# Kernel optimization log

Hardware: AMD Instinct MI355X
Metric: run time of the kernel (lower is better)

The kernel has to match this reference:

```python
import jax, jax.numpy as jnp
import numpy as np

B, N, C, H, W = 8, 512, 3, 16, 16
K, P, E = 2, 4, 1           # K: hop levels == filter taps, P: attn heads, E: edge feature sets
SLOPE = 0.2                 # LeakyReLU slope in attention
GAT_DIMS = {'d0': (128, 128), 'd1': (512, 32), 'u0': (128, 64),
            'u1': (256, 128), 's0': (128, 128), 's1': (512, 64)}


def _conv(x, w, b):
    pad = w.shape[-1] // 2
    y = jax.lax.conv_general_dilated(x, w, (1, 1), [(pad, pad), (pad, pad)],
                                     dimension_numbers=('NCHW', 'OIHW', 'NCHW'))
    return y + b[None, :, None, None]


def _gat(x, S, wk, wq, wf, b):
    # x: (B,G,N); S: (B,E,N,N) binary GSO. KeyQuery attention + K-tap attentional filter.
    key = jnp.einsum('pegf,bgn->bpefn', wk, x)
    qry = jnp.einsum('pegf,bgn->bpefn', wq, x)
    # scores[...,n,m]: logit of node n attending to neighbor m
    scores = jax.nn.leaky_relu(jnp.einsum('bpefn,bpefm->bpenm', qry, key), SLOPE)
    mask = (jnp.abs(S) > 1e-9)[:, None]                    # (B,1,E,N,N)
    aij = jnp.where(mask, jax.nn.softmax(jnp.where(mask, scores, -1e9), axis=-1), 0.0)
    Pn, En, Kt, G, F = wf.shape
    xk = jnp.broadcast_to(x[:, None, None], (x.shape[0], Pn, En, G, x.shape[-1]))
    zs = [xk]
    for _ in range(Kt - 1):
        xk = jnp.einsum('bpegm,bpenm->bpegn', xk, aij)     # attention-weighted diffusion
        zs.append(xk)
    z = jnp.stack(zs, axis=3)                              # (B,P,E,K,G,N)
    y = jnp.einsum('bpekgn,pekgf->bpfn', z, wf) + b[None, None, :, None]
    y = jax.nn.relu(y)                                     # nonlinearity before head concat
    return y.reshape(y.shape[0], Pn * F, y.shape[-1])      # (B, P*F, N)


def _forward(x, Slist, conv0_w, conv0_b, conv1_w, conv1_b, flat_w, flat_b,
             d0_wk, d0_wq, d0_wf, d0_b, d1_wk, d1_wq, d1_wf, d1_b,
             u0_wk, u0_wq, u0_wf, u0_b, u1_wk, u1_wq, u1_wf, u1_b,
             s0_wk, s0_wq, s0_wf, s0_b, s1_wk, s1_wq, s1_wf, s1_b,
             dec0_w, dec0_b, dec1_w, dec1_b):
    Bn, Nn = x.shape[0], x.shape[1]
    h = x.reshape(Bn * Nn, C, H, W)
    e = jax.nn.relu(_conv(h, conv0_w, conv0_b))
    e = jax.nn.relu(_conv(e, conv1_w, conv1_b))
    e = e + h                                              # RES connection after encoder
    f = jax.nn.relu(e.reshape(Bn * Nn, -1) @ flat_w.T + flat_b)
    g = f.reshape(Bn, -1, Nn)                              # faithful torch reshape to (B, F, N)
    S0, S1 = Slist[:, 0:1], Slist[:, 1:2]
    p0 = g
    p1 = _gat(p0, S0, d0_wk, d0_wq, d0_wf, d0_b)           # downward pass
    p2 = _gat(p1, S1, d1_wk, d1_wq, d1_wf, d1_b)
    # upward pass + shortcuts (upward[l] uses S[K-l-1]; shortcut[K-1-l] on p[K-1-l])
    u0 = _gat(p2, S1, u0_wk, u0_wq, u0_wf, u0_b) + _gat(p1, S1, s1_wk, s1_wq, s1_wf, s1_b)
    u1 = _gat(u0, S0, u1_wk, u1_wq, u1_wf, u1_b) + _gat(p0, S0, s0_wk, s0_wq, s0_wf, s0_b)
    d = jax.nn.relu(u1.reshape(Bn * Nn, -1) @ dec0_w.T + dec0_b)
    out = jax.nn.softmax(d @ dec1_w.T + dec1_b, axis=-1)   # nn.Softmax() -> dim=1 on 2D input
    return out.reshape(Bn, Nn, -1)


def setup_inputs() -> dict:
    key = jax.random.key(0)
    ks = iter(jax.random.split(key, 64))
    def nrm(shape, s=0.1):
        return jax.random.normal(next(ks), shape, jnp.float32) * s
    x = jax.random.normal(next(ks), (B, N, C, H, W), jnp.float32)
    adj = (jax.random.uniform(next(ks), (B, K, N, N)) < 0.02).astype(jnp.float32)
    Slist = jnp.clip(adj + jnp.eye(N, dtype=jnp.float32)[None, None], 0.0, 1.0)
    inp = {'x': x, 'Slist': Slist,
           'conv0_w': nrm((32, C, 3, 3)), 'conv0_b': nrm((32,)),
           'conv1_w': nrm((C, 32, 3, 3)), 'conv1_b': nrm((C,)),
           'flat_w': nrm((128, C * H * W)), 'flat_b': nrm((128,))}
    for pre, (G, F) in GAT_DIMS.items():
        inp[pre + '_wk'] = nrm((P, E, G, F))
        inp[pre + '_wq'] = nrm((P, E, G, F))
        inp[pre + '_wf'] = nrm((P, E, K, G, F))
        inp[pre + '_b'] = nrm((F,))
    inp.update({'dec0_w': nrm((256, 512)), 'dec0_b': nrm((256,)),
                'dec1_w': nrm((5, 256)), 'dec1_b': nrm((5,))})
    return inp


def reference(x, Slist, conv0_w, conv0_b, conv1_w, conv1_b, flat_w, flat_b,
              d0_wk, d0_wq, d0_wf, d0_b, d1_wk, d1_wq, d1_wf, d1_b,
              u0_wk, u0_wq, u0_wf, u0_b, u1_wk, u1_wq, u1_wf, u1_b,
              s0_wk, s0_wq, s0_wf, s0_b, s1_wk, s1_wq, s1_wf, s1_b,
              dec0_w, dec0_b, dec1_w, dec1_b):
    return _forward(x, Slist, conv0_w, conv0_b, conv1_w, conv1_b, flat_w, flat_b,
                    d0_wk, d0_wq, d0_wf, d0_b, d1_wk, d1_wq, d1_wf, d1_b,
                    u0_wk, u0_wq, u0_wf, u0_b, u1_wk, u1_wq, u1_wf, u1_b,
                    s0_wk, s0_wq, s0_wf, s0_b, s1_wk, s1_wq, s1_wf, s1_b,
                    dec0_w, dec0_b, dec1_w, dec1_b)
```

## Files before the change

kernel.cpp:

```cpp
#include <hip/hip_runtime.h>
#include <hip/hip_bf16.h>
#include <math.h>

typedef unsigned short u16;
typedef unsigned int   u32;

#define CAP 48

__device__ __forceinline__ float tof(u16 u){
  union { u32 i; float f; } v; v.i = ((u32)u) << 16; return v.f;
}
__device__ __forceinline__ u16 fromf(float f){
  union { float f; u32 i; } v; v.f = f;
  u32 x = v.i;
  return (u16)((x + 0x7fffu + ((x >> 16) & 1u)) >> 16);
}

__global__ void detect_dtype(const void* xp, int* flag){
  if(threadIdx.x == 0 && blockIdx.x == 0){
    const u16* p = (const u16*)xp;
    int outl = 0;
    for(int i = 0; i < 128; i++){
      u16 u = p[2*i];
      int e = (u >> 7) & 0xFF;
      if(u != 0 && (e < 100 || e > 140)) outl++;
    }
    *flag = (outl > 32) ? 1 : 0;
  }
}

struct WArgs {
  const void* p[34];
  int sz[34];
  int off[35];
};

__global__ __launch_bounds__(256) void convert_weights(WArgs wa, const int* flag,
                                                       float* __restrict__ arena, int total){
  int i = blockIdx.x * 256 + threadIdx.x;
  if(i >= total) return;
  int isf = *flag;
  int t = 0;
  while(wa.off[t+1] <= i) t++;
  int j = i - wa.off[t];
  float v = 0.f;
  if(j < wa.sz[t])
    v = isf ? ((const float*)wa.p[t])[j] : tof(((const u16*)wa.p[t])[j]);
  arena[i] = v;
}

__global__ __launch_bounds__(256) void transpose_w(const float* __restrict__ src,
                                                   float* __restrict__ dst, int R, int C){
  int i = blockIdx.x * 256 + threadIdx.x;
  if(i < R*C){
    int r = i / C, c = i - r*C;
    dst[(size_t)c*R + r] = src[i];
  }
}

__global__ __launch_bounds__(64) void build_nbr(const void* __restrict__ S,
                                                int* __restrict__ nbr_idx,
                                                int* __restrict__ nbr_cnt,
                                                const int* __restrict__ flag){
  int isf = *flag;
  int row  = blockIdx.x;
  int lane = threadIdx.x;
  int cnt = 0;
  for(int c = 0; c < 8; c++){
    int m = c*64 + lane;
    size_t idx = (size_t)row * 512 + m;
    float sv = isf ? ((const float*)S)[idx] : tof(((const u16*)S)[idx]);
    bool pred = fabsf(sv) > 1e-9f;
    unsigned long long mask = __ballot(pred);
    int pos = cnt + __popcll(mask & ((1ull << lane) - 1ull));
    if(pred && pos < CAP) nbr_idx[(size_t)row*CAP + pos] = m;
    cnt += __popcll(mask);
  }
  if(lane == 0) nbr_cnt[row] = cnt > CAP ? CAP : cnt;
}

__global__ __launch_bounds__(256) void encoder_conv(
    const void* __restrict__ x, const int* __restrict__ flag,
    const float* __restrict__ w0, const float* __restrict__ b0,
    const float* __restrict__ w1, const float* __restrict__ b1,
    float* __restrict__ e1n)
{
  __shared__ float xpad[3][18][18];
  __shared__ float e0p[16][18][18];

  int isf = *flag;
  int tid = threadIdx.x;
  size_t img = blockIdx.x;
  int py = tid >> 4, px = tid & 15;

  float* z1 = &xpad[0][0][0];
  for(int i = tid; i < 972; i += 256) z1[i] = 0.f;
  float* z2 = &e0p[0][0][0];
  for(int i = tid; i < 5184; i += 256) z2[i] = 0.f;
  __syncthreads();

  #pragma unroll
  for(int i = 0; i < 3; i++){
    size_t gi = img*768 + i*256 + tid;
    xpad[i][1+py][1+px] = isf ? ((const float*)x)[gi] : tof(((const u16*)x)[gi]);
  }
  __syncthreads();

  float acc1[3] = {0.f, 0.f, 0.f};

  for(int grp = 0; grp < 2; grp++){
    float acc0[16];
    #pragma unroll
    for(int o = 0; o < 16; o++) acc0[o] = 0.f;
    for(int i = 0; i < 3; i++){
      float rr[9];
      #pragma unroll
      for(int ky = 0; ky < 3; ky++)
        #pragma unroll
        for(int kx = 0; kx < 3; kx++)
          rr[ky*3+kx] = xpad[i][py+ky][px+kx];
      #pragma unroll
      for(int o = 0; o < 16; o++){
        #pragma unroll
        for(int t = 0; t < 9; t++)
          acc0[o] = fmaf(rr[t], w0[(grp*16+o)*27 + i*9 + t], acc0[o]);
      }
    }
    __syncthreads();
    #pragma unroll
    for(int o = 0; o < 16; o++)
      e0p[o][1+py][1+px] = fmaxf(acc0[o] + b0[grp*16 + o], 0.f);
    __syncthreads();

    for(int i = 0; i < 16; i++){
      float rr[9];
      #pragma unroll
      for(int ky = 0; ky < 3; ky++)
        #pragma unroll
        for(int kx = 0; kx < 3; kx++)
          rr[ky*3+kx] = e0p[i][py+ky][px+kx];
      int ic = grp*16 + i;
      #pragma unroll
      for(int o = 0; o < 3; o++){
        #pragma unroll
        for(int t = 0; t < 9; t++)
          acc1[o] = fmaf(rr[t], w1[o*288 + ic*9 + t], acc1[o]);
      }
    }
  }

  #pragma unroll
  for(int o = 0; o < 3; o++)
    e1n[img*768 + o*256 + tid] = fmaxf(acc1[o] + b1[o], 0.f) + xpad[o][1+py][1+px];
}

__global__ __launch_bounds__(256) void gemm_flat(
    const float* __restrict__ e1n, const float* __restrict__ fwT,
    const float* __restrict__ fb, float* __restrict__ g)
{
  __shared__ float As[16][68];
  __shared__ float Bs[16][68];
  int tid = threadIdx.x;
  int n0 = blockIdx.x * 64, m0 = blockIdx.y * 64;

  int lk = tid >> 4;
  int l4 = (tid & 15) * 4;
  int br = tid >> 2;
  int bc = (tid & 3) * 4;

  float acc[4][4];
  #pragma unroll
  for(int i = 0; i < 4; i++)
    #pragma unroll
    for(int jj = 0; jj < 4; jj++) acc[i][jj] = 0.f;

  int tm = tid >> 4, tn = tid & 15;
  for(int kt = 0; kt < 48; kt++){
    int k0 = kt*16;
    *(float4*)&As[lk][l4] = *(const float4*)&fwT[(size_t)(k0 + lk)*128 + m0 + l4];
    float4 bv = *(const float4*)&e1n[(size_t)(n0 + br)*768 + k0 + bc];
    Bs[bc+0][br] = bv.x; Bs[bc+1][br] = bv.y; Bs[bc+2][br] = bv.z; Bs[bc+3][br] = bv.w;
    __syncthreads();
    #pragma unroll
    for(int kk = 0; kk < 16; kk++){
      float4 a  = *(const float4*)&As[kk][tm*4];
      float4 xx = *(const float4*)&Bs[kk][tn*4];
      float av[4]  = {a.x, a.y, a.z, a.w};
      float xvv[4] = {xx.x, xx.y, xx.z, xx.w};
      #pragma unroll
      for(int i = 0; i < 4; i++)
        #pragma unroll
        for(int jj = 0; jj < 4; jj++)
          acc[i][jj] = fmaf(av[i], xvv[jj], acc[i][jj]);
    }
    __syncthreads();
  }

  #pragma unroll
  for(int jj = 0; jj < 4; jj++){
    int img = n0 + tn*4 + jj;
    float4 r = make_float4(fmaxf(acc[0][jj] + fb[m0+tm*4+0], 0.f),
                           fmaxf(acc[1][jj] + fb[m0+tm*4+1], 0.f),
                           fmaxf(acc[2][jj] + fb[m0+tm*4+2], 0.f),
                           fmaxf(acc[3][jj] + fb[m0+tm*4+3], 0.f));
    *(float4*)&g[(size_t)img*128 + m0 + tm*4] = r;
  }
}

__global__ __launch_bounds__(256) void gemm_kq(
    const float* __restrict__ X,
    const float* __restrict__ wk, const float* __restrict__ wq,
    float* __restrict__ kqT, int G, int F)
{
  __shared__ float Ws[32][68];
  __shared__ float Xs[32][68];
  int tid = threadIdx.x;
  int bp = blockIdx.z;
  int b = bp >> 2, p = bp & 3;
  int n0 = blockIdx.x * 64, m0 = blockIdx.y * 64;
  const float* Xb = X + (size_t)b * G * 512;

  int lk = tid >> 4;
  int l4 = (tid & 15) * 4;

  int mg = m0 + l4;
  int quad = mg / F;
  int mq = mg - quad * F;
  size_t GF = (size_t)G * F;
  const float* wb = (quad == 0 ? wk : wq) + (size_t)p * GF + mq;

  float acc[4][4];
  #pragma unroll
  for(int i = 0; i < 4; i++)
    #pragma unroll
    for(int jj = 0; jj < 4; jj++) acc[i][jj] = 0.f;

  int tm = tid >> 4, tn = tid & 15;
  int KT = G / 32;
  for(int kt = 0; kt < KT; kt++){
    int k = kt*32 + lk;
    *(float4*)&Ws[lk][l4]      = *(const float4*)(wb + (size_t)k * F);
    *(float4*)&Ws[lk+16][l4]   = *(const float4*)(wb + (size_t)(k+16) * F);
    *(float4*)&Xs[lk][l4]      = *(const float4*)(Xb + (size_t)k * 512 + n0 + l4);
    *(float4*)&Xs[lk+16][l4]   = *(const float4*)(Xb + (size_t)(k+16) * 512 + n0 + l4);
    __syncthreads();
    #pragma unroll
    for(int kk = 0; kk < 32; kk++){
      float4 a  = *(const float4*)&Ws[kk][tm*4];
      float4 xx = *(const float4*)&Xs[kk][tn*4];
      float av[4]  = {a.x, a.y, a.z, a.w};
      float xvv[4] = {xx.x, xx.y, xx.z, xx.w};
      #pragma unroll
      for(int i = 0; i < 4; i++)
        #pragma unroll
        for(int jj = 0; jj < 4; jj++)
          acc[i][jj] = fmaf(av[i], xvv[jj], acc[i][jj]);
    }
    __syncthreads();
  }

  int F2 = 2*F;
  float* ob = kqT + (size_t)bp * 512 * F2;
  #pragma unroll
  for(int jj = 0; jj < 4; jj++){
    float* orow = ob + (size_t)(n0 + tn*4 + jj) * F2 + m0 + tm*4;
    #pragma unroll
    for(int i = 0; i < 4; i++) orow[i] = acc[i][jj];
  }
}

__global__ __launch_bounds__(256) void gemm_kqK64(
    const float* __restrict__ X,
    const float* __restrict__ wk, const float* __restrict__ wq,
    float* __restrict__ kqT, int G, int F)
{
  __shared__ float Ws[64][68];
  __shared__ float Xs[64][68];
  int tid = threadIdx.x;
  int bp = blockIdx.z;
  int b = bp >> 2, p = bp & 3;
  int n0 = blockIdx.x * 64, m0 = blockIdx.y * 64;
  const float* Xb = X + (size_t)b * G * 512;

  int lk = tid >> 4;
  int l4 = (tid & 15) * 4;

  int mg = m0 + l4;
  int quad = mg / F;
  int mq = mg - quad * F;
  size_t GF = (size_t)G * F;
  const float* wb = (quad == 0 ? wk : wq) + (size_t)p * GF + mq;

  float acc[4][4];
  #pragma unroll
  for(int i = 0; i < 4; i++)
    #pragma unroll
    for(int jj = 0; jj < 4; jj++) acc[i][jj] = 0.f;

  int tm = tid >> 4, tn = tid & 15;
  int KT = G / 64;
  for(int kt = 0; kt < KT; kt++){
    #pragma unroll
    for(int kb = 0; kb < 4; kb++){
      int k = kt*64 + lk + kb*16;
      *(float4*)&Ws[lk + kb*16][l4] = *(const float4*)(wb + (size_t)k * F);
      *(float4*)&Xs[lk + kb*16][l4] = *(const float4*)(Xb + (size_t)k * 512 + n0 + l4);
    }
    __syncthreads();
    #pragma unroll
    for(int kk = 0; kk < 64; kk++){
      float4 a  = *(const float4*)&Ws[kk][tm*4];
      float4 xx = *(const float4*)&Xs[kk][tn*4];
      float av[4]  = {a.x, a.y, a.z, a.w};
      float xvv[4] = {xx.x, xx.y, xx.z, xx.w};
      #pragma unroll
      for(int i = 0; i < 4; i++)
        #pragma unroll
        for(int jj = 0; jj < 4; jj++)
          acc[i][jj] = fmaf(av[i], xvv[jj], acc[i][jj]);
    }
    __syncthreads();
  }

  int F2 = 2*F;
  float* ob = kqT + (size_t)bp * 512 * F2;
  #pragma unroll
  for(int jj = 0; jj < 4; jj++){
    float* orow = ob + (size_t)(n0 + tn*4 + jj) * F2 + m0 + tm*4;
    #pragma unroll
    for(int i = 0; i < 4; i++) orow[i] = acc[i][jj];
  }
}

__global__ __launch_bounds__(256) void attn_sparse(
    const float* __restrict__ kqT,
    const int* __restrict__ nbr_idx, const int* __restrict__ nbr_cnt,
    float* __restrict__ aijv, int F, int s)
{
  __shared__ float qs[16][132];
  __shared__ float sc[16][CAP];
  __shared__ float red[16][2];
  int tid = threadIdx.x;
  int n0 = blockIdx.x * 16;
  int bp = blockIdx.y;
  int b = bp >> 2;
  int F2 = 2*F;

  int F4 = F >> 2;
  for(int i = tid; i < 16*F4; i += 256){
    int r = i / F4, c4 = (i - r*F4) * 4;
    *(float4*)&qs[r][c4] =
      *(const float4*)&kqT[((size_t)bp*512 + n0 + r)*F2 + F + c4];
  }
  __syncthreads();

  int r = tid >> 4;
  int t = tid & 15;
  int n = n0 + r;
  int srow = (b*2 + s)*512 + n;
  int cnt = nbr_cnt[srow];
  const int* il = nbr_idx + (size_t)srow * CAP;

  for(int j = t; j < cnt; j += 16){
    int m = il[j];
    const float* krow = kqT + ((size_t)bp*512 + m)*F2;
    float a = 0.f;
    for(int f = 0; f < F; f += 4){
      float4 k4 = *(const float4*)&krow[f];
      a = fmaf(qs[r][f],   k4.x, a);
      a = fmaf(qs[r][f+1], k4.y, a);
      a = fmaf(qs[r][f+2], k4.z, a);
      a = fmaf(qs[r][f+3], k4.w, a);
    }
    sc[r][j] = a >= 0.f ? a : 0.2f * a;
  }
  __syncthreads();

  if(t == 0){
    float mx = -1e30f;
    for(int j = 0; j < cnt; j++) mx = fmaxf(mx, sc[r][j]);
    float ssum = 0.f;
    for(int j = 0; j < cnt; j++) ssum += expf(sc[r][j] - mx);
    red[r][0] = mx; red[r][1] = ssum;
  }
  __syncthreads();

  float mx = red[r][0], ssum = red[r][1];
  float* arow = aijv + ((size_t)bp*512 + n)*CAP;
  for(int j = t; j < cnt; j += 16)
    arow[j] = expf(sc[r][j] - mx) / ssum;
}

__global__ __launch_bounds__(256) void fill_Xp(
    const float* __restrict__ X, const float* __restrict__ aijv,
    const int* __restrict__ nbr_idx, const int* __restrict__ nbr_cnt,
    float* __restrict__ Xp, int G, int s)
{
  __shared__ float xrows[8][512];
  __shared__ float av_s[64][CAP+1];
  __shared__ u16   il_s[64][CAP+2];
  __shared__ int   cnt_s[64];

  int tid = threadIdx.x;
  int n0 = blockIdx.x * 64;
  int g0 = blockIdx.y * 32;
  int bp = blockIdx.z;
  int b = bp >> 2;
  int srow0 = (b*2 + s)*512 + n0;

  for(int i = tid; i < 64*CAP; i += 256){
    int r = i / CAP, j = i - r*CAP;
    il_s[r][j] = (u16)nbr_idx[(size_t)(srow0 + r)*CAP + j];
    av_s[r][j] = aijv[((size_t)bp*512 + n0 + r)*CAP + j];
  }
  if(tid < 64) cnt_s[tid] = nbr_cnt[srow0 + tid];

  int n_l = tid & 63;
  int gs  = tid >> 6;
  const float* Xb  = X  + ((size_t)b  * G + g0) * 512;
  float*       XpB = Xp + ((size_t)bp * G + g0) * 512;

  for(int gb = 0; gb < 32; gb += 8){
    __syncthreads();
    for(int i = tid; i < 8*128; i += 256){
      int gr = i >> 7, c4 = (i & 127) * 4;
      *(float4*)&xrows[gr][c4] = *(const float4*)&Xb[(size_t)(gb + gr)*512 + c4];
    }
    __syncthreads();
    int cnt = cnt_s[n_l];
    float a0 = 0.f, a1 = 0.f;
    for(int j = 0; j < cnt; j++){
      float w = av_s[n_l][j];
      int   m = il_s[n_l][j];
      a0 = fmaf(w, xrows[gs][m],     a0);
      a1 = fmaf(w, xrows[gs + 4][m], a1);
    }
    XpB[(size_t)(gb + gs)*512     + n0 + n_l] = a0;
    XpB[(size_t)(gb + gs + 4)*512 + n0 + n_l] = a1;
  }
}

__global__ __launch_bounds__(256) void gemm_y(
    const float* __restrict__ X, const float* __restrict__ Xp,
    const float* __restrict__ wf, const float* __restrict__ bias,
    float* __restrict__ out, int G, int F, int PFout, int accmode)
{
  __shared__ float Ws[32][68];
  __shared__ float Xs[32][68];
  int tid = threadIdx.x;
  int bp = blockIdx.z;
  int b = bp >> 2, p = bp & 3;
  int n0 = blockIdx.x * 64, m0 = blockIdx.y * 64;

  int lk = tid >> 4;
  int l4 = (tid & 15) * 4;
  int mg = m0 + l4;
  int fcl = mg < F ? mg : (F - 4);
  size_t GF2 = (size_t)2 * G * F;
  const float* wb = wf + (size_t)p * GF2 + fcl;

  float acc[4][4];
  #pragma unroll
  for(int i = 0; i < 4; i++)
    #pragma unroll
    for(int jj = 0; jj < 4; jj++) acc[i][jj] = 0.f;

  int tm = tid >> 4, tn = tid & 15;
  int KT = (2*G) / 32;
  for(int kt = 0; kt < KT; kt++){
    int c0 = kt*32 + lk;
    int c1 = c0 + 16;
    const float* xr0 = (c0 < G) ? (X  + ((size_t)b  * G + c0      ) * 512)
                                : (Xp + ((size_t)bp * G + (c0 - G)) * 512);
    const float* xr1 = (c1 < G) ? (X  + ((size_t)b  * G + c1      ) * 512)
                                : (Xp + ((size_t)bp * G + (c1 - G)) * 512);
    *(float4*)&Ws[lk][l4]    = *(const float4*)(wb + (size_t)c0 * F);
    *(float4*)&Ws[lk+16][l4] = *(const float4*)(wb + (size_t)c1 * F);
    *(float4*)&Xs[lk][l4]    = *(const float4*)(xr0 + n0 + l4);
    *(float4*)&Xs[lk+16][l4] = *(const float4*)(xr1 + n0 + l4);
    __syncthreads();
    #pragma unroll
    for(int kk = 0; kk < 32; kk++){
      float4 a  = *(const float4*)&Ws[kk][tm*4];
      float4 xx = *(const float4*)&Xs[kk][tn*4];
      float av[4]  = {a.x, a.y, a.z, a.w};
      float xvv[4] = {xx.x, xx.y, xx.z, xx.w};
      #pragma unroll
      for(int i = 0; i < 4; i++)
        #pragma unroll
        for(int jj = 0; jj < 4; jj++)
          acc[i][jj] = fmaf(av[i], xvv[jj], acc[i][jj]);
    }
    __syncthreads();
  }

  int mrow = m0 + tm*4;
  if(mrow < F){
    float* ob = out + ((size_t)b * PFout + (size_t)p * F + mrow) * 512 + n0 + tn*4;
    #pragma unroll
    for(int i = 0; i < 4; i++){
      float bv = bias[mrow + i];
      float4 r = make_float4(fmaxf(acc[i][0] + bv, 0.f),
                             fmaxf(acc[i][1] + bv, 0.f),
                             fmaxf(acc[i][2] + bv, 0.f),
                             fmaxf(acc[i][3] + bv, 0.f));
      float* dst = ob + (size_t)i * 512;
      if(accmode){
        float4 old = *(float4*)dst;
        r.x += old.x; r.y += old.y; r.z += old.z; r.w += old.w;
      }
      *(float4*)dst = r;
    }
  }
}

__global__ __launch_bounds__(256) void gemm_yK64(
    const float* __restrict__ X, const float* __restrict__ Xp,
    const float* __restrict__ wf, const float* __restrict__ bias,
    float* __restrict__ out, int G, int F, int PFout, int accmode)
{
  __shared__ float Ws[64][68];
  __shared__ float Xs[64][68];
  int tid = threadIdx.x;
  int bp = blockIdx.z;
  int b = bp >> 2, p = bp & 3;
  int n0 = blockIdx.x * 64, m0 = blockIdx.y * 64;

  int lk = tid >> 4;
  int l4 = (tid & 15) * 4;
  int mg = m0 + l4;
  int fcl = mg < F ? mg : (F - 4);
  size_t GF2 = (size_t)2 * G * F;
  const float* wb = wf + (size_t)p * GF2 + fcl;

  float acc[4][4];
  #pragma unroll
  for(int i = 0; i < 4; i++)
    #pragma unroll
    for(int jj = 0; jj < 4; jj++) acc[i][jj] = 0.f;

  int tm = tid >> 4, tn = tid & 15;
  int KT = (2*G) / 64;
  for(int kt = 0; kt < KT; kt++){
    #pragma unroll
    for(int kb = 0; kb < 4; kb++){
      int c = kt*64 + lk + kb*16;
      const float* xr = (c < G) ? (X  + ((size_t)b  * G + c      ) * 512)
                                : (Xp + ((size_t)bp * G + (c - G)) * 512);
      *(float4*)&Ws[lk + kb*16][l4] = *(const float4*)(wb + (size_t)c * F);
      *(float4*)&Xs[lk + kb*16][l4] = *(const float4*)(xr + n0 + l4);
    }
    __syncthreads();
    #pragma unroll
    for(int kk = 0; kk < 64; kk++){
      float4 a  = *(const float4*)&Ws[kk][tm*4];
      float4 xx = *(const float4*)&Xs[kk][tn*4];
      float av[4]  = {a.x, a.y, a.z, a.w};
      float xvv[4] = {xx.x, xx.y, xx.z, xx.w};
      #pragma unroll
      for(int i = 0; i < 4; i++)
        #pragma unroll
        for(int jj = 0; jj < 4; jj++)
          acc[i][jj] = fmaf(av[i], xvv[jj], acc[i][jj]);
    }
    __syncthreads();
  }

  int mrow = m0 + tm*4;
  if(mrow < F){
    float* ob = out + ((size_t)b * PFout + (size_t)p * F + mrow) * 512 + n0 + tn*4;
    #pragma unroll
    for(int i = 0; i < 4; i++){
      float bv = bias[mrow + i];
      float4 r = make_float4(fmaxf(acc[i][0] + bv, 0.f),
                             fmaxf(acc[i][1] + bv, 0.f),
                             fmaxf(acc[i][2] + bv, 0.f),
                             fmaxf(acc[i][3] + bv, 0.f));
      float* dst = ob + (size_t)i * 512;
      if(accmode){
        float4 old = *(float4*)dst;
        r.x += old.x; r.y += old.y; r.z += old.z; r.w += old.w;
      }
      *(float4*)dst = r;
    }
  }
}

__global__ __launch_bounds__(256) void gemm_dec0(
    const float* __restrict__ u1, const float* __restrict__ w0T,
    const float* __restrict__ b0, float* __restrict__ d)
{
  __shared__ float As[16][68];
  __shared__ float Bs[16][68];
  int tid = threadIdx.x;
  int n0 = blockIdx.x * 64;
  int m0 = blockIdx.y * 64;

  int lk = tid >> 4;
  int l4 = (tid & 15) * 4;
  int br = tid >> 2;
  int bc = (tid & 3) * 4;

  float acc[4][4];
  #pragma unroll
  for(int i = 0; i < 4; i++)
    #pragma unroll
    for(int jj = 0; jj < 4; jj++) acc[i][jj] = 0.f;

  int tm = tid >> 4, tn = tid & 15;
  for(int kt = 0; kt < 32; kt++){
    int k0 = kt*16;
    *(float4*)&As[lk][l4] = *(const float4*)&w0T[(size_t)(k0 + lk)*256 + m0 + l4];
    float4 bv = *(const float4*)&u1[(size_t)(n0 + br)*512 + k0 + bc];
    Bs[bc+0][br] = bv.x; Bs[bc+1][br] = bv.y; Bs[bc+2][br] = bv.z; Bs[bc+3][br] = bv.w;
    __syncthreads();
    #pragma unroll
    for(int kk = 0; kk < 16; kk++){
      float4 a  = *(const float4*)&As[kk][tm*4];
      float4 xx = *(const float4*)&Bs[kk][tn*4];
      float av[4]  = {a.x, a.y, a.z, a.w};
      float xvv[4] = {xx.x, xx.y, xx.z, xx.w};
      #pragma unroll
      for(int i = 0; i < 4; i++)
        #pragma unroll
        for(int jj = 0; jj < 4; jj++)
          acc[i][jj] = fmaf(av[i], xvv[jj], acc[i][jj]);
    }
    __syncthreads();
  }

  #pragma unroll
  for(int jj = 0; jj < 4; jj++){
    int row = n0 + tn*4 + jj;
    float4 r = make_float4(fmaxf(acc[0][jj] + b0[m0+tm*4+0], 0.f),
                           fmaxf(acc[1][jj] + b0[m0+tm*4+1], 0.f),
                           fmaxf(acc[2][jj] + b0[m0+tm*4+2], 0.f),
                           fmaxf(acc[3][jj] + b0[m0+tm*4+3], 0.f));
    *(float4*)&d[(size_t)row*256 + m0 + tm*4] = r;
  }
}

__global__ __launch_bounds__(64) void decoder2(
    const float* __restrict__ d,
    const float* __restrict__ w1, const float* __restrict__ b1,
    const int* __restrict__ flag, void* __restrict__ outp)
{
  __shared__ float ds[256];
  __shared__ float lg[5];
  int r = blockIdx.x, lane = threadIdx.x;
  for(int i = lane; i < 256; i += 64) ds[i] = d[(size_t)r*256 + i];
  __syncthreads();

  if(lane < 5){
    float a = 0.f;
    const float* wr = w1 + (size_t)lane * 256;
    for(int i = 0; i < 256; i++) a = fmaf(ds[i], wr[i], a);
    lg[lane] = a + b1[lane];
  }
  __syncthreads();
  if(lane < 5){
    float mx = lg[0];
    for(int i = 1; i < 5; i++) mx = fmaxf(mx, lg[i]);
    float ssum = 0.f;
    for(int i = 0; i < 5; i++) ssum += expf(lg[i] - mx);
    float v = expf(lg[lane] - mx) / ssum;
    if(*flag) ((float*)outp)[(size_t)r*5 + lane] = v;
    else      ((u16*)outp)[(size_t)r*5 + lane] = fromf(v);
  }
}

extern "C" void kernel_launch(void* const* d_in, const int* in_sizes, int n_in,
                              void* d_out, int out_size, void* d_ws, size_t ws_size,
                              hipStream_t stream)
{
  (void)n_in; (void)out_size; (void)ws_size;
  const void* x = d_in[0];
  const void* S = d_in[1];

  float* wsf   = (float*)d_ws;
  int*   flag  = (int*)d_ws;
  float* arena = wsf + 1024;

  WArgs wa;
  long long aoff[35]; aoff[0] = 0;
  for(int t = 0; t < 34; t++){
    wa.p[t]  = d_in[2 + t];
    wa.sz[t] = in_sizes[2 + t];
    wa.off[t] = (int)aoff[t];
    aoff[t+1] = aoff[t] + ((in_sizes[2 + t] + 15) & ~15);
  }
  wa.off[34] = (int)aoff[34];
  int total = (int)aoff[34];

  size_t cur = 1024 + (size_t)((total + 1023) & ~1023);
  float* g    = wsf + cur; cur += 524288;
  float* p1   = wsf + cur; cur += 2097152;
  float* p2   = wsf + cur; cur += 524288;
  float* u0b  = wsf + cur; cur += 1048576;
  float* u1b  = p1;
  float* scr  = wsf + cur; cur += (size_t)32*512*512;
  float* aijv = wsf + cur; cur += (size_t)32*512*CAP;
  float* fwT  = wsf + cur; cur += 98304;
  float* dw0T = wsf + cur; cur += 131072;
  int*   ncnt = (int*)(wsf + cur); cur += 8192;
  int*   nidx = (int*)(wsf + cur); cur += (size_t)8192 * CAP;

  float* e1n = scr;
  float* kqT = scr;
  float* Xp  = scr;
  float* dbuf= scr;

  const float* A[34];
  for(int t = 0; t < 34; t++) A[t] = arena + aoff[t];
  const float* c0w = A[0], *c0b = A[1], *c1w = A[2], *c1b = A[3];
  const float* fw  = A[4], *fb  = A[5];
  const float *wk_[6], *wq_[6], *wf_[6], *bias_[6];
  for(int l = 0; l < 6; l++){
    wk_[l]   = A[6 + 4*l];
    wq_[l]   = A[7 + 4*l];
    wf_[l]   = A[8 + 4*l];
    bias_[l] = A[9 + 4*l];
  }
  const float* dw0 = A[30], *db0 = A[31], *dw1 = A[32], *db1 = A[33];

  detect_dtype<<<1, 64, 0, stream>>>(x, flag);
  convert_weights<<<(total + 255)/256, 256, 0, stream>>>(wa, flag, arena, total);
  transpose_w<<<(98304 + 255)/256, 256, 0, stream>>>(fw, fwT, 128, 768);
  transpose_w<<<(131072 + 255)/256, 256, 0, stream>>>(dw0, dw0T, 256, 512);
  build_nbr<<<8192, 64, 0, stream>>>(S, nidx, ncnt, flag);
  encoder_conv<<<4096, 256, 0, stream>>>(x, flag, c0w, c0b, c1w, c1b, e1n);
  gemm_flat<<<dim3(64, 2), 256, 0, stream>>>(e1n, fwT, fb, g);

  struct Lyr { int G, F, s; const float* in; float* out; int PF; int acc; int w; };
  const Lyr Ls[6] = {
    {128, 128, 0, g,   p1,  512, 0, 0},
    {512,  32, 1, p1,  p2,  128, 0, 1},
    {128,  64, 1, p2,  u0b, 256, 0, 2},
    {512,  64, 1, p1,  u0b, 256, 1, 5},
    {256, 128, 0, u0b, u1b, 512, 0, 3},
    {128, 128, 0, g,   u1b, 512, 1, 4},
  };
  for(int i = 0; i < 6; i++){
    const Lyr& L = Ls[i];
    if(2*L.F <= 64){
      dim3 gk(8, 1, 32);
      gemm_kqK64<<<gk, 256, 0, stream>>>(L.in, wk_[L.w], wq_[L.w], kqT, L.G, L.F);
    } else {
      dim3 gk(8, (2*L.F)/64, 32);
      gemm_kq<<<gk, 256, 0, stream>>>(L.in, wk_[L.w], wq_[L.w], kqT, L.G, L.F);
    }
    attn_sparse<<<dim3(32, 32), 256, 0, stream>>>(kqT, nidx, ncnt, aijv, L.F, L.s);
    fill_Xp<<<dim3(8, L.G/32, 32), 256, 0, stream>>>(L.in, aijv, nidx, ncnt, Xp, L.G, L.s);
    if(L.F <= 64){
      dim3 gy(8, 1, 32);
      gemm_yK64<<<gy, 256, 0, stream>>>(L.in, Xp, wf_[L.w], bias_[L.w], L.out,
                                        L.G, L.F, L.PF, L.acc);
    } else {
      dim3 gy(8, (L.F + 63)/64, 32);
      gemm_y<<<gy, 256, 0, stream>>>(L.in, Xp, wf_[L.w], bias_[L.w], L.out,
                                     L.G, L.F, L.PF, L.acc);
    }
  }

  gemm_dec0<<<dim3(64, 4), 256, 0, stream>>>(u1b, dw0T, db0, dbuf);
  decoder2<<<4096, 64, 0, stream>>>(dbuf, dw1, db1, flag, d_out);
}
```

Before: 980.8 us.

## Batch independent GAT layer pairs into shared kernel launches

```diff
diff --git a/kernel.cpp b/kernel.cpp
--- a/kernel.cpp
+++ b/kernel.cpp
@@ -207,27 +207,30 @@
   }
 }
 
-__global__ __launch_bounds__(256) void gemm_kq(
-    const float* __restrict__ X,
-    const float* __restrict__ wk, const float* __restrict__ wq,
-    float* __restrict__ kqT, int G, int F)
-{
-  __shared__ float Ws[32][68];
-  __shared__ float Xs[32][68];
+struct KqP { const float* X; const float* wk; const float* wq; float* kqT;
+             int G, F, my; };
+
+__global__ __launch_bounds__(256) void gemm_kq2(KqP A, KqP B)
+{
+  __shared__ float Ws[32*68];
+  __shared__ float Xs[32*68];
   int tid = threadIdx.x;
+  int by = blockIdx.y;
+  KqP P = (by < A.my) ? A : B;
+  int lby = (by < A.my) ? by : (by - A.my);
   int bp = blockIdx.z;
   int b = bp >> 2, p = bp & 3;
-  int n0 = blockIdx.x * 64, m0 = blockIdx.y * 64;
-  const float* Xb = X + (size_t)b * G * 512;
+  int n0 = blockIdx.x * 64, m0 = lby * 64;
+  const float* Xb = P.X + (size_t)b * P.G * 512;
 
   int lk = tid >> 4;
   int l4 = (tid & 15) * 4;
 
   int mg = m0 + l4;
-  int quad = mg / F;
-  int mq = mg - quad * F;
-  size_t GF = (size_t)G * F;
-  const float* wb = (quad == 0 ? wk : wq) + (size_t)p * GF + mq;
+  int quad = mg / P.F;
+  int mq = mg - quad * P.F;
+  size_t GF = (size_t)P.G * P.F;
+  const float* wb = (quad == 0 ? P.wk : P.wq) + (size_t)p * GF + mq;
 
   float acc[4][4];
   #pragma unroll
@@ -236,18 +239,18 @@
     for(int jj = 0; jj < 4; jj++) acc[i][jj] = 0.f;
 
   int tm = tid >> 4, tn = tid & 15;
-  int KT = G / 32;
+  int KT = P.G / 32;
   for(int kt = 0; kt < KT; kt++){
     int k = kt*32 + lk;
-    *(float4*)&Ws[lk][l4]      = *(const float4*)(wb + (size_t)k * F);
-    *(float4*)&Ws[lk+16][l4]   = *(const float4*)(wb + (size_t)(k+16) * F);
-    *(float4*)&Xs[lk][l4]      = *(const float4*)(Xb + (size_t)k * 512 + n0 + l4);
-    *(float4*)&Xs[lk+16][l4]   = *(const float4*)(Xb + (size_t)(k+16) * 512 + n0 + l4);
+    *(float4*)&Ws[lk*68 + l4]      = *(const float4*)(wb + (size_t)k * P.F);
+    *(float4*)&Ws[(lk+16)*68 + l4] = *(const float4*)(wb + (size_t)(k+16) * P.F);
+    *(float4*)&Xs[lk*68 + l4]      = *(const float4*)(Xb + (size_t)k * 512 + n0 + l4);
+    *(float4*)&Xs[(lk+16)*68 + l4] = *(const float4*)(Xb + (size_t)(k+16) * 512 + n0 + l4);
     __syncthreads();
     #pragma unroll
     for(int kk = 0; kk < 32; kk++){
-      float4 a  = *(const float4*)&Ws[kk][tm*4];
-      float4 xx = *(const float4*)&Xs[kk][tn*4];
+      float4 a  = *(const float4*)&Ws[kk*68 + tm*4];
+      float4 xx = *(const float4*)&Xs[kk*68 + tn*4];
       float av[4]  = {a.x, a.y, a.z, a.w};
       float xvv[4] = {xx.x, xx.y, xx.z, xx.w};
       #pragma unroll
@@ -259,8 +262,8 @@
     __syncthreads();
   }
 
-  int F2 = 2*F;
-  float* ob = kqT + (size_t)bp * 512 * F2;
+  int F2 = 2*P.F;
+  float* ob = P.kqT + (size_t)bp * 512 * F2;
   #pragma unroll
   for(int jj = 0; jj < 4; jj++){
     float* orow = ob + (size_t)(n0 + tn*4 + jj) * F2 + m0 + tm*4;
@@ -332,10 +335,11 @@
   }
 }
 
-__global__ __launch_bounds__(256) void attn_sparse(
-    const float* __restrict__ kqT,
-    const int* __restrict__ nbr_idx, const int* __restrict__ nbr_cnt,
-    float* __restrict__ aijv, int F, int s)
+struct AtP { const float* kqT; float* aijv; int F, s; };
+
+__global__ __launch_bounds__(256) void attn2(
+    AtP A, AtP B,
+    const int* __restrict__ nbr_idx, const int* __restrict__ nbr_cnt)
 {
   __shared__ float qs[16][132];
   __shared__ float sc[16][CAP];
@@ -343,8 +347,11 @@
   int tid = threadIdx.x;
   int n0 = blockIdx.x * 16;
   int bp = blockIdx.y;
+  AtP P = (blockIdx.z == 0) ? A : B;
   int b = bp >> 2;
+  int F = P.F;
   int F2 = 2*F;
+  const float* kqT = P.kqT;
 
   int F4 = F >> 2;
   for(int i = tid; i < 16*F4; i += 256){
@@ -357,7 +364,7 @@
   int r = tid >> 4;
   int t = tid & 15;
   int n = n0 + r;
-  int srow = (b*2 + s)*512 + n;
+  int srow = (b*2 + P.s)*512 + n;
   int cnt = nbr_cnt[srow];
   const int* il = nbr_idx + (size_t)srow * CAP;
 
@@ -386,15 +393,16 @@
   __syncthreads();
 
   float mx = red[r][0], ssum = red[r][1];
-  float* arow = aijv + ((size_t)bp*512 + n)*CAP;
+  float* arow = P.aijv + ((size_t)bp*512 + n)*CAP;
   for(int j = t; j < cnt; j += 16)
     arow[j] = expf(sc[r][j] - mx) / ssum;
 }
 
-__global__ __launch_bounds__(256) void fill_Xp(
-    const float* __restrict__ X, const float* __restrict__ aijv,
-    const int* __restrict__ nbr_idx, const int* __restrict__ nbr_cnt,
-    float* __restrict__ Xp, int G, int s)
+struct FiP { const float* X; const float* aijv; float* Xp; int G, s, gy; };
+
+__global__ __launch_bounds__(256) void fill_Xp2(
+    FiP A, FiP B,
+    const int* __restrict__ nbr_idx, const int* __restrict__ nbr_cnt)
 {
   __shared__ float xrows[8][512];
   __shared__ float av_s[64][CAP+1];
@@ -402,23 +410,26 @@
   __shared__ int   cnt_s[64];
 
   int tid = threadIdx.x;
+  int by = blockIdx.y;
+  FiP P = (by < A.gy) ? A : B;
+  int lby = (by < A.gy) ? by : (by - A.gy);
   int n0 = blockIdx.x * 64;
-  int g0 = blockIdx.y * 32;
+  int g0 = lby * 32;
   int bp = blockIdx.z;
   int b = bp >> 2;
-  int srow0 = (b*2 + s)*512 + n0;
+  int srow0 = (b*2 + P.s)*512 + n0;
 
   for(int i = tid; i < 64*CAP; i += 256){
     int r = i / CAP, j = i - r*CAP;
     il_s[r][j] = (u16)nbr_idx[(size_t)(srow0 + r)*CAP + j];
-    av_s[r][j] = aijv[((size_t)bp*512 + n0 + r)*CAP + j];
+    av_s[r][j] = P.aijv[((size_t)bp*512 + n0 + r)*CAP + j];
   }
   if(tid < 64) cnt_s[tid] = nbr_cnt[srow0 + tid];
 
   int n_l = tid & 63;
   int gs  = tid >> 6;
-  const float* Xb  = X  + ((size_t)b  * G + g0) * 512;
-  float*       XpB = Xp + ((size_t)bp * G + g0) * 512;
+  const float* Xb  = P.X  + ((size_t)b  * P.G + g0) * 512;
+  float*       XpB = P.Xp + ((size_t)bp * P.G + g0) * 512;
 
   for(int gb = 0; gb < 32; gb += 8){
     __syncthreads();
@@ -440,24 +451,28 @@
   }
 }
 
-__global__ __launch_bounds__(256) void gemm_y(
-    const float* __restrict__ X, const float* __restrict__ Xp,
-    const float* __restrict__ wf, const float* __restrict__ bias,
-    float* __restrict__ out, int G, int F, int PFout, int accmode)
-{
-  __shared__ float Ws[32][68];
-  __shared__ float Xs[32][68];
+struct YP { const float* X; const float* Xp; const float* wf; const float* bias;
+            float* out; int G, F, PF, acc, my; };
+
+__global__ __launch_bounds__(256) void gemm_y2_32(YP A, YP B)
+{
+  __shared__ float Ws[32*68];
+  __shared__ float Xs[32*68];
   int tid = threadIdx.x;
+  int by = blockIdx.y;
+  YP P = (by < A.my) ? A : B;
+  int lby = (by < A.my) ? by : (by - A.my);
   int bp = blockIdx.z;
   int b = bp >> 2, p = bp & 3;
-  int n0 = blockIdx.x * 64, m0 = blockIdx.y * 64;
+  int n0 = blockIdx.x * 64, m0 = lby * 64;
+  int G = P.G, F = P.F;
 
   int lk = tid >> 4;
   int l4 = (tid & 15) * 4;
   int mg = m0 + l4;
   int fcl = mg < F ? mg : (F - 4);
   size_t GF2 = (size_t)2 * G * F;
-  const float* wb = wf + (size_t)p * GF2 + fcl;
+  const float* wb = P.wf + (size_t)p * GF2 + fcl;
 
   float acc[4][4];
   #pragma unroll
@@ -470,19 +485,19 @@
   for(int kt = 0; kt < KT; kt++){
     int c0 = kt*32 + lk;
     int c1 = c0 + 16;
-    const float* xr0 = (c0 < G) ? (X  + ((size_t)b  * G + c0      ) * 512)
-                                : (Xp + ((size_t)bp * G + (c0 - G)) * 512);
-    const float* xr1 = (c1 < G) ? (X  + ((size_t)b  * G + c1      ) * 512)
-                                : (Xp + ((size_t)bp * G + (c1 - G)) * 512);
-    *(float4*)&Ws[lk][l4]    = *(const float4*)(wb + (size_t)c0 * F);
-    *(float4*)&Ws[lk+16][l4] = *(const float4*)(wb + (size_t)c1 * F);
-    *(float4*)&Xs[lk][l4]    = *(const float4*)(xr0 + n0 + l4);
-    *(float4*)&Xs[lk+16][l4] = *(const float4*)(xr1 + n0 + l4);
+    const float* xr0 = (c0 < G) ? (P.X  + ((size_t)b  * G + c0      ) * 512)
+                                : (P.Xp + ((size_t)bp * G + (c0 - G)) * 512);
+    const float* xr1 = (c1 < G) ? (P.X  + ((size_t)b  * G + c1      ) * 512)
+                                : (P.Xp + ((size_t)bp * G + (c1 - G)) * 512);
+    *(float4*)&Ws[lk*68 + l4]      = *(const float4*)(wb + (size_t)c0 * F);
+    *(float4*)&Ws[(lk+16)*68 + l4] = *(const float4*)(wb + (size_t)c1 * F);
+    *(float4*)&Xs[lk*68 + l4]      = *(const float4*)(xr0 + n0 + l4);
+    *(float4*)&Xs[(lk+16)*68 + l4] = *(const float4*)(xr1 + n0 + l4);
     __syncthreads();
     #pragma unroll
     for(int kk = 0; kk < 32; kk++){
-      float4 a  = *(const float4*)&Ws[kk][tm*4];
-      float4 xx = *(const float4*)&Xs[kk][tn*4];
+      float4 a  = *(const float4*)&Ws[kk*68 + tm*4];
+      float4 xx = *(const float4*)&Xs[kk*68 + tn*4];
       float av[4]  = {a.x, a.y, a.z, a.w};
       float xvv[4] = {xx.x, xx.y, xx.z, xx.w};
       #pragma unroll
@@ -496,16 +511,16 @@
 
   int mrow = m0 + tm*4;
   if(mrow < F){
-    float* ob = out + ((size_t)b * PFout + (size_t)p * F + mrow) * 512 + n0 + tn*4;
+    float* ob = P.out + ((size_t)b * P.PF + (size_t)p * F + mrow) * 512 + n0 + tn*4;
     #pragma unroll
     for(int i = 0; i < 4; i++){
-      float bv = bias[mrow + i];
+      float bv = P.bias[mrow + i];
       float4 r = make_float4(fmaxf(acc[i][0] + bv, 0.f),
                              fmaxf(acc[i][1] + bv, 0.f),
                              fmaxf(acc[i][2] + bv, 0.f),
                              fmaxf(acc[i][3] + bv, 0.f));
       float* dst = ob + (size_t)i * 512;
-      if(accmode){
+      if(P.acc){
         float4 old = *(float4*)dst;
         r.x += old.x; r.y += old.y; r.z += old.z; r.w += old.w;
       }
@@ -514,24 +529,25 @@
   }
 }
 
-__global__ __launch_bounds__(256) void gemm_yK64(
-    const float* __restrict__ X, const float* __restrict__ Xp,
-    const float* __restrict__ wf, const float* __restrict__ bias,
-    float* __restrict__ out, int G, int F, int PFout, int accmode)
-{
-  __shared__ float Ws[64][68];
-  __shared__ float Xs[64][68];
+__global__ __launch_bounds__(256) void gemm_y2_K64(YP A, YP B)
+{
+  __shared__ float Ws[64*68];
+  __shared__ float Xs[64*68];
   int tid = threadIdx.x;
+  int by = blockIdx.y;
+  YP P = (by < A.my) ? A : B;
+  int lby = (by < A.my) ? by : (by - A.my);
   int bp = blockIdx.z;
   int b = bp >> 2, p = bp & 3;
-  int n0 = blockIdx.x * 64, m0 = blockIdx.y * 64;
+  int n0 = blockIdx.x * 64, m0 = lby * 64;
+  int G = P.G, F = P.F;
 
   int lk = tid >> 4;
   int l4 = (tid & 15) * 4;
   int mg = m0 + l4;
   int fcl = mg < F ? mg : (F - 4);
   size_t GF2 = (size_t)2 * G * F;
-  const float* wb = wf + (size_t)p * GF2 + fcl;
+  const float* wb = P.wf + (size_t)p * GF2 + fcl;
 
   float acc[4][4];
   #pragma unroll
@@ -545,16 +561,16 @@
     #pragma unroll
     for(int kb = 0; kb < 4; kb++){
       int c = kt*64 + lk + kb*16;
-      const float* xr = (c < G) ? (X  + ((size_t)b  * G + c      ) * 512)
-                                : (Xp + ((size_t)bp * G + (c - G)) * 512);
-      *(float4*)&Ws[lk + kb*16][l4] = *(const float4*)(wb + (size_t)c * F);
-      *(float4*)&Xs[lk + kb*16][l4] = *(const float4*)(xr + n0 + l4);
+      const float* xr = (c < G) ? (P.X  + ((size_t)b  * G + c      ) * 512)
+                                : (P.Xp + ((size_t)bp * G + (c - G)) * 512);
+      *(float4*)&Ws[(lk + kb*16)*68 + l4] = *(const float4*)(wb + (size_t)c * F);
+      *(float4*)&Xs[(lk + kb*16)*68 + l4] = *(const float4*)(xr + n0 + l4);
     }
     __syncthreads();
     #pragma unroll
     for(int kk = 0; kk < 64; kk++){
-      float4 a  = *(const float4*)&Ws[kk][tm*4];
-      float4 xx = *(const float4*)&Xs[kk][tn*4];
+      float4 a  = *(const float4*)&Ws[kk*68 + tm*4];
+      float4 xx = *(const float4*)&Xs[kk*68 + tn*4];
       float av[4]  = {a.x, a.y, a.z, a.w};
       float xvv[4] = {xx.x, xx.y, xx.z, xx.w};
       #pragma unroll
@@ -568,21 +584,32 @@
 
   int mrow = m0 + tm*4;
   if(mrow < F){
-    float* ob = out + ((size_t)b * PFout + (size_t)p * F + mrow) * 512 + n0 + tn*4;
+    float* ob = P.out + ((size_t)b * P.PF + (size_t)p * F + mrow) * 512 + n0 + tn*4;
     #pragma unroll
     for(int i = 0; i < 4; i++){
-      float bv = bias[mrow + i];
+      float bv = P.bias[mrow + i];
       float4 r = make_float4(fmaxf(acc[i][0] + bv, 0.f),
                              fmaxf(acc[i][1] + bv, 0.f),
                              fmaxf(acc[i][2] + bv, 0.f),
                              fmaxf(acc[i][3] + bv, 0.f));
       float* dst = ob + (size_t)i * 512;
-      if(accmode){
+      if(P.acc){
         float4 old = *(float4*)dst;
         r.x += old.x; r.y += old.y; r.z += old.z; r.w += old.w;
       }
       *(float4*)dst = r;
     }
+  }
+}
+
+__global__ __launch_bounds__(256) void add_vec(float* __restrict__ dst,
+                                               const float* __restrict__ src, int n4){
+  int i = blockIdx.x * 256 + threadIdx.x;
+  if(i < n4){
+    float4 a = ((const float4*)dst)[i];
+    float4 b = ((const float4*)src)[i];
+    a.x += b.x; a.y += b.y; a.z += b.z; a.w += b.w;
+    ((float4*)dst)[i] = a;
   }
 }
 
@@ -697,18 +724,31 @@
   float* p1   = wsf + cur; cur += 2097152;
   float* p2   = wsf + cur; cur += 524288;
   float* u0b  = wsf + cur; cur += 1048576;
+  float* u0c  = wsf + cur; cur += 1048576;
+  float* u1c  = wsf + cur; cur += 2097152;
   float* u1b  = p1;
-  float* scr  = wsf + cur; cur += (size_t)32*512*512;
-  float* aijv = wsf + cur; cur += (size_t)32*512*CAP;
+  float* aijvA= wsf + cur; cur += (size_t)32*512*CAP;
+  float* aijvB= wsf + cur; cur += (size_t)32*512*CAP;
   float* fwT  = wsf + cur; cur += 98304;
   float* dw0T = wsf + cur; cur += 131072;
   int*   ncnt = (int*)(wsf + cur); cur += 8192;
   int*   nidx = (int*)(wsf + cur); cur += (size_t)8192 * CAP;
-
-  float* e1n = scr;
-  float* kqT = scr;
-  float* Xp  = scr;
-  float* dbuf= scr;
+  float* pool = wsf + cur; cur += 10485760;
+
+  float* e1n   = pool;
+  float* kqT0  = pool;
+  float* Xp0   = pool;
+  float* kqT1  = pool;
+  float* Xp1   = pool;
+  float* kqT2  = pool;
+  float* kqT3  = pool + 2097152;
+  float* Xp2   = pool;
+  float* Xp3   = pool + 2097152;
+  float* kqT4  = pool;
+  float* kqT5  = pool + 4194304;
+  float* Xp4   = pool;
+  float* Xp5   = pool + 4194304;
+  float* dbuf  = pool;
 
   const float* A[34];
   for(int t = 0; t < 34; t++) A[t] = arena + aoff[t];
@@ -731,35 +771,57 @@
   encoder_conv<<<4096, 256, 0, stream>>>(x, flag, c0w, c0b, c1w, c1b, e1n);
   gemm_flat<<<dim3(64, 2), 256, 0, stream>>>(e1n, fwT, fb, g);
 
-  struct Lyr { int G, F, s; const float* in; float* out; int PF; int acc; int w; };
-  const Lyr Ls[6] = {
-    {128, 128, 0, g,   p1,  512, 0, 0},
-    {512,  32, 1, p1,  p2,  128, 0, 1},
-    {128,  64, 1, p2,  u0b, 256, 0, 2},
-    {512,  64, 1, p1,  u0b, 256, 1, 5},
-    {256, 128, 0, u0b, u1b, 512, 0, 3},
-    {128, 128, 0, g,   u1b, 512, 1, 4},
-  };
-  for(int i = 0; i < 6; i++){
-    const Lyr& L = Ls[i];
-    if(2*L.F <= 64){
-      dim3 gk(8, 1, 32);
-      gemm_kqK64<<<gk, 256, 0, stream>>>(L.in, wk_[L.w], wq_[L.w], kqT, L.G, L.F);
-    } else {
-      dim3 gk(8, (2*L.F)/64, 32);
-      gemm_kq<<<gk, 256, 0, stream>>>(L.in, wk_[L.w], wq_[L.w], kqT, L.G, L.F);
-    }
-    attn_sparse<<<dim3(32, 32), 256, 0, stream>>>(kqT, nidx, ncnt, aijv, L.F, L.s);
-    fill_Xp<<<dim3(8, L.G/32, 32), 256, 0, stream>>>(L.in, aijv, nidx, ncnt, Xp, L.G, L.s);
-    if(L.F <= 64){
-      dim3 gy(8, 1, 32);
-      gemm_yK64<<<gy, 256, 0, stream>>>(L.in, Xp, wf_[L.w], bias_[L.w], L.out,
-                                        L.G, L.F, L.PF, L.acc);
-    } else {
-      dim3 gy(8, (L.F + 63)/64, 32);
-      gemm_y<<<gy, 256, 0, stream>>>(L.in, Xp, wf_[L.w], bias_[L.w], L.out,
-                                     L.G, L.F, L.PF, L.acc);
-    }
+  {
+    KqP k0 = { g, wk_[0], wq_[0], kqT0, 128, 128, 4 };
+    gemm_kq2<<<dim3(8, 4, 32), 256, 0, stream>>>(k0, k0);
+    AtP a0 = { kqT0, aijvA, 128, 0 };
+    attn2<<<dim3(32, 32, 1), 256, 0, stream>>>(a0, a0, nidx, ncnt);
+    FiP f0 = { g, aijvA, Xp0, 128, 0, 4 };
+    fill_Xp2<<<dim3(8, 4, 32), 256, 0, stream>>>(f0, f0, nidx, ncnt);
+    YP y0 = { g, Xp0, wf_[0], bias_[0], p1, 128, 128, 512, 0, 2 };
+    gemm_y2_32<<<dim3(8, 2, 32), 256, 0, stream>>>(y0, y0);
+  }
+
+  {
+    gemm_kqK64<<<dim3(8, 1, 32), 256, 0, stream>>>(p1, wk_[1], wq_[1], kqT1, 512, 32);
+    AtP a1 = { kqT1, aijvA, 32, 1 };
+    attn2<<<dim3(32, 32, 1), 256, 0, stream>>>(a1, a1, nidx, ncnt);
+    FiP f1 = { p1, aijvA, Xp1, 512, 1, 16 };
+    fill_Xp2<<<dim3(8, 16, 32), 256, 0, stream>>>(f1, f1, nidx, ncnt);
+    YP y1 = { p1, Xp1, wf_[1], bias_[1], p2, 512, 32, 128, 0, 1 };
+    gemm_y2_K64<<<dim3(8, 1, 32), 256, 0, stream>>>(y1, y1);
+  }
+
+  {
+    KqP k2 = { p2, wk_[2], wq_[2], kqT2, 128, 64, 2 };
+    KqP k3 = { p1, wk_[5], wq_[5], kqT3, 512, 64, 2 };
+    gemm_kq2<<<dim3(8, 4, 32), 256, 0, stream>>>(k2, k3);
+    AtP a2 = { kqT2, aijvA, 64, 1 };
+    AtP a3 = { kqT3, aijvB, 64, 1 };
+    attn2<<<dim3(32, 32, 2), 256, 0, stream>>>(a2, a3, nidx, ncnt);
+    FiP f2 = { p2, aijvA, Xp2, 128, 1, 4 };
+    FiP f3 = { p1, aijvB, Xp3, 512, 1, 16 };
+    fill_Xp2<<<dim3(8, 20, 32), 256, 0, stream>>>(f2, f3, nidx, ncnt);
+    YP y2 = { p2, Xp2, wf_[2], bias_[2], u0b, 128, 64, 256, 0, 1 };
+    YP y3 = { p1, Xp3, wf_[5], bias_[5], u0c, 512, 64, 256, 0, 1 };
+    gemm_y2_K64<<<dim3(8, 2, 32), 256, 0, stream>>>(y2, y3);
+    add_vec<<<1024, 256, 0, stream>>>(u0b, u0c, 262144);
+  }
+
+  {
+    KqP k4 = { u0b, wk_[3], wq_[3], kqT4, 256, 128, 4 };
+    KqP k5 = { g,   wk_[4], wq_[4], kqT5, 128, 128, 4 };
+    gemm_kq2<<<dim3(8, 8, 32), 256, 0, stream>>>(k4, k5);
+    AtP a4 = { kqT4, aijvA, 128, 0 };
+    AtP a5 = { kqT5, aijvB, 128, 0 };
+    attn2<<<dim3(32, 32, 2), 256, 0, stream>>>(a4, a5, nidx, ncnt);
+    FiP f4 = { u0b, aijvA, Xp4, 256, 0, 8 };
+    FiP f5 = { g,   aijvB, Xp5, 128, 0, 4 };
+    fill_Xp2<<<dim3(8, 12, 32), 256, 0, stream>>>(f4, f5, nidx, ncnt);
+    YP y4 = { u0b, Xp4, wf_[3], bias_[3], u1b, 256, 128, 512, 0, 2 };
+    YP y5 = { g,   Xp5, wf_[4], bias_[4], u1c, 128, 128, 512, 0, 2 };
+    gemm_y2_32<<<dim3(8, 4, 32), 256, 0, stream>>>(y4, y5);
+    add_vec<<<2048, 256, 0, stream>>>(u1b, u1c, 524288);
   }
 
   gemm_dec0<<<dim3(64, 4), 256, 0, stream>>>(u1b, dw0T, db0, dbuf);
```

New measurement: 961.2 us. 1.02x faster.
